# Optimization experiments

Hardware: AMD Instinct MI355X
Metric: run time of the kernel (lower is better)

## Reference

```python
import jax, jax.numpy as jnp
import numpy as np

NUM_HEADS = 32
HEAD_DIM = 128
LORA_RANK = 512
Q_LORA_RANK = 1536
BSZ = 16
SEQ_LEN = 4096


def setup_inputs() -> dict:
    key = jax.random.key(0)
    k1, k2, k3, k4, k5, k6 = jax.random.split(key, 6)
    hd = NUM_HEADS * HEAD_DIM
    return {
        "hidden_states_q": jax.random.normal(k1, (BSZ, Q_LORA_RANK), dtype=jnp.float32),
        "compressed_kv": jax.random.normal(k2, (BSZ, SEQ_LEN, LORA_RANK), dtype=jnp.float32),
        # nn.Linear params: weight [out, in], bias [out]
        "Wq": jax.random.normal(k3, (hd, Q_LORA_RANK), dtype=jnp.float32) / np.sqrt(Q_LORA_RANK),
        "bq": jax.random.normal(k4, (hd,), dtype=jnp.float32) * 0.01,
        "Wkv": jax.random.normal(k5, (hd, LORA_RANK), dtype=jnp.float32) / np.sqrt(LORA_RANK),
        "bkv": jax.random.normal(k6, (hd,), dtype=jnp.float32) * 0.01,
    }


def reference(hidden_states_q, compressed_kv, Wq, bq, Wkv, bkv):
    bsz = hidden_states_q.shape[0]
    seq_len = compressed_kv.shape[1]
    # q: [b, h, d]
    q = (hidden_states_q @ Wq.T + bq).reshape(bsz, NUM_HEADS, HEAD_DIM)
    # kv decompression: [b, s, h, d] (same tensor used for both K and V)
    kv = (compressed_kv @ Wkv.T + bkv).reshape(bsz, seq_len, NUM_HEADS, HEAD_DIM)
    # attention scores per head over seq (note: original has NO 1/sqrt(d) scaling)
    attn = jnp.einsum('bhd,bshd->bhs', q, kv)
    attn = jax.nn.softmax(attn, axis=-1)
    out = jnp.einsum('bhs,bshd->bhd', attn, kv)
    return out.reshape(bsz, NUM_HEADS * HEAD_DIM)
```

## Files before the change

kernel.cpp:

```cpp
#include <hip/hip_runtime.h>

#define B  16
#define S  4096
#define R  512
#define QR 1536
#define H  32
#define D  128
#define HD 4096
#define SC 128
#define CH 32

using f32x4 = __attribute__((ext_vector_type(4))) float;
using s16x8 = __attribute__((ext_vector_type(8))) short;

__device__ __forceinline__ ushort bf_hi(float x) {
  return (ushort)(__float_as_uint(x) >> 16);
}
__device__ __forceinline__ float bf_res(float x) {
  return x - __uint_as_float(__float_as_uint(x) & 0xFFFF0000u);
}
__device__ __forceinline__ ushort f2bf_rne(float x) {
  uint u = __float_as_uint(x);
  return (ushort)((u + 0x7FFFu + ((u >> 16) & 1u)) >> 16);
}
__device__ __forceinline__ float bf2f(ushort u) {
  return __uint_as_float((uint)u << 16);
}

__global__ __launch_bounds__(512) void k_q(const float* __restrict__ hsq,
                                           const float* __restrict__ Wq,
                                           const float* __restrict__ bq,
                                           float* __restrict__ q) {
  __shared__ float hs[B * QR];
  int tid = threadIdx.x;
  for (int idx = tid * 4; idx < B * QR; idx += 2048)
    *(float4*)&hs[idx] = *(const float4*)&hsq[idx];
  __syncthreads();

  int wave = tid >> 6, lane = tid & 63;
  int o = blockIdx.x * 16 + wave * 2;

  float acc0[B], acc1[B];
#pragma unroll
  for (int b = 0; b < B; ++b) { acc0[b] = 0.f; acc1[b] = 0.f; }

  const float* w0r = Wq + (size_t)o * QR;
  const float* w1r = w0r + QR;
  for (int k = lane * 4; k < QR; k += 256) {
    float4 wa = *(const float4*)&w0r[k];
    float4 wb = *(const float4*)&w1r[k];
#pragma unroll
    for (int b = 0; b < B; ++b) {
      float4 h4 = *(const float4*)&hs[b * QR + k];
      acc0[b] += wa.x * h4.x + wa.y * h4.y + wa.z * h4.z + wa.w * h4.w;
      acc1[b] += wb.x * h4.x + wb.y * h4.y + wb.z * h4.z + wb.w * h4.w;
    }
  }
#pragma unroll
  for (int b = 0; b < B; ++b) {
    float v0 = acc0[b], v1 = acc1[b];
#pragma unroll
    for (int off = 32; off > 0; off >>= 1) {
      v0 += __shfl_xor(v0, off);
      v1 += __shfl_xor(v1, off);
    }
    if (lane == 0) {
      q[b * HD + o]     = v0 + bq[o];
      q[b * HD + o + 1] = v1 + bq[o + 1];
    }
  }
}

__global__ __launch_bounds__(256) void k_qhat(const float* __restrict__ q,
                                              const float* __restrict__ Wkv,
                                              float* __restrict__ qhat) {
  int h = blockIdx.x;
  int r0 = blockIdx.y * 64;
  __shared__ float qs[B][D];
  int tid = threadIdx.x;
  for (int idx = tid; idx < B * D; idx += 256) {
    int b = idx >> 7, d = idx & (D - 1);
    qs[b][d] = q[b * HD + h * D + d];
  }
  __syncthreads();

  int r_l = tid & 63, bg = tid >> 6;
  float acc[4] = {0.f, 0.f, 0.f, 0.f};
  const float* wbase = Wkv + (size_t)(h * D) * R + r0 + r_l;
  for (int d = 0; d < D; d += 4) {
    float w0 = wbase[(d + 0) * R];
    float w1 = wbase[(d + 1) * R];
    float w2 = wbase[(d + 2) * R];
    float w3 = wbase[(d + 3) * R];
#pragma unroll
    for (int i = 0; i < 4; ++i) {
      float4 q4 = *(const float4*)&qs[bg * 4 + i][d];
      acc[i] += q4.x * w0 + q4.y * w1 + q4.z * w2 + q4.w * w3;
    }
  }
#pragma unroll
  for (int i = 0; i < 4; ++i)
    qhat[((size_t)(bg * 4 + i) * H + h) * R + r0 + r_l] = acc[i];
}

__global__ __launch_bounds__(512, 4) void k_fmha(const float* __restrict__ qhat,
                                                 const float* __restrict__ ckv,
                                                 ushort* __restrict__ part,
                                                 float* __restrict__ mbuf,
                                                 float* __restrict__ lbuf) {
  __shared__ __align__(16) ushort smem[24576];
  __shared__ __align__(16) ushort Ps[H * 128];

  ushort* cs1h = smem;
  ushort* cs1l = smem + 8192;
  ushort* qsh  = smem + 16384;
  ushort* qsl  = smem + 20480;
  float*  redm = (float*)(smem + 8192);
  float*  redl = redm + 256;
  ushort* cs2  = smem;

  const int b = blockIdx.x, chunk = blockIdx.y;
  const int tid = threadIdx.x;
  const int lane = tid & 63, w = tid >> 6;
  const int lcol = lane & 15, lgrp = lane >> 4;
  const float* cbase = ckv + ((size_t)b * S + (size_t)chunk * SC) * R;
  const float* qbase = qhat + (size_t)b * H * R;

  const int st_s = tid >> 2;
  const int st_k = (tid & 3) * 16;
  const int qrow = tid >> 4;
  const int qk   = (tid & 15) * 4;

  f32x4 acc[2];
  acc[0] = {0.f, 0.f, 0.f, 0.f};
  acc[1] = {0.f, 0.f, 0.f, 0.f};

  float4 v[4], vq;
  {
    const float* src = cbase + (size_t)st_s * R + st_k;
#pragma unroll
    for (int j = 0; j < 4; ++j) v[j] = *(const float4*)(src + 4 * j);
    vq = *(const float4*)(qbase + (size_t)qrow * R + qk);
  }

  for (int kt = 0; kt < R; kt += 64) {
#pragma unroll
    for (int j = 0; j < 4; ++j) {
      int k0 = st_k + 4 * j;
      int idx = st_s * 64 + (((k0 >> 3) ^ (st_s & 7)) << 3) + (k0 & 7);
      float4 t = v[j];
      *(uint*)&cs1h[idx]     = (uint)bf_hi(t.x) | ((uint)bf_hi(t.y) << 16);
      *(uint*)&cs1h[idx + 2] = (uint)bf_hi(t.z) | ((uint)bf_hi(t.w) << 16);
      *(uint*)&cs1l[idx]     = (uint)bf_hi(bf_res(t.x)) | ((uint)bf_hi(bf_res(t.y)) << 16);
      *(uint*)&cs1l[idx + 2] = (uint)bf_hi(bf_res(t.z)) | ((uint)bf_hi(bf_res(t.w)) << 16);
    }
    {
      int idx = qrow * 64 + (((qk >> 3) ^ (qrow & 7)) << 3) + (qk & 7);
      *(uint*)&qsh[idx]     = (uint)bf_hi(vq.x) | ((uint)bf_hi(vq.y) << 16);
      *(uint*)&qsh[idx + 2] = (uint)bf_hi(vq.z) | ((uint)bf_hi(vq.w) << 16);
      *(uint*)&qsl[idx]     = (uint)bf_hi(bf_res(vq.x)) | ((uint)bf_hi(bf_res(vq.y)) << 16);
      *(uint*)&qsl[idx + 2] = (uint)bf_hi(bf_res(vq.z)) | ((uint)bf_hi(bf_res(vq.w)) << 16);
    }
    __syncthreads();
    if (kt + 64 < R) {
      const float* src = cbase + (size_t)st_s * R + (kt + 64) + st_k;
#pragma unroll
      for (int j = 0; j < 4; ++j) v[j] = *(const float4*)(src + 4 * j);
      vq = *(const float4*)(qbase + (size_t)qrow * R + (kt + 64) + qk);
    }
#pragma unroll
    for (int ks = 0; ks < 2; ++ks) {
      const int kb = ks * 4 + lgrp;
      s16x8 ah[2], al[2], bh, bl;
#pragma unroll
      for (int mt = 0; mt < 2; ++mt) {
        int m = 16 * mt + lcol;
        int idx = m * 64 + ((kb ^ (m & 7)) << 3);
        ah[mt] = *(s16x8*)&qsh[idx];
        al[mt] = *(s16x8*)&qsl[idx];
      }
      {
        int sf = 16 * w + lcol;
        int idx = sf * 64 + ((kb ^ (sf & 7)) << 3);
        bh = *(s16x8*)&cs1h[idx];
        bl = *(s16x8*)&cs1l[idx];
      }
#pragma unroll
      for (int mt = 0; mt < 2; ++mt) {
        acc[mt] = __builtin_amdgcn_mfma_f32_16x16x32_bf16(ah[mt], bh, acc[mt], 0, 0, 0);
        acc[mt] = __builtin_amdgcn_mfma_f32_16x16x32_bf16(ah[mt], bl, acc[mt], 0, 0, 0);
        acc[mt] = __builtin_amdgcn_mfma_f32_16x16x32_bf16(al[mt], bh, acc[mt], 0, 0, 0);
      }
    }
    __syncthreads();
  }

  float pm[2][4];
#pragma unroll
  for (int mt = 0; mt < 2; ++mt)
#pragma unroll
    for (int i = 0; i < 4; ++i) pm[mt][i] = acc[mt][i];
#pragma unroll
  for (int off = 1; off <= 8; off <<= 1)
#pragma unroll
    for (int mt = 0; mt < 2; ++mt)
#pragma unroll
      for (int i = 0; i < 4; ++i)
        pm[mt][i] = fmaxf(pm[mt][i], __shfl_xor(pm[mt][i], off));
  if (lcol == 0) {
#pragma unroll
    for (int mt = 0; mt < 2; ++mt)
#pragma unroll
      for (int i = 0; i < 4; ++i)
        redm[(16 * mt + lgrp * 4 + i) * 8 + w] = pm[mt][i];
  }
  __syncthreads();

  float e_[2][4], ps[2][4];
#pragma unroll
  for (int mt = 0; mt < 2; ++mt)
#pragma unroll
    for (int i = 0; i < 4; ++i) {
      int h = 16 * mt + lgrp * 4 + i;
      float4 r0 = *(float4*)&redm[h * 8];
      float4 r1 = *(float4*)&redm[h * 8 + 4];
      float m = fmaxf(fmaxf(fmaxf(r0.x, r0.y), fmaxf(r0.z, r0.w)),
                      fmaxf(fmaxf(r1.x, r1.y), fmaxf(r1.z, r1.w)));
      float e = __expf(acc[mt][i] - m);
      e_[mt][i] = e;
      ps[mt][i] = e;
    }
#pragma unroll
  for (int off = 1; off <= 8; off <<= 1)
#pragma unroll
    for (int mt = 0; mt < 2; ++mt)
#pragma unroll
      for (int i = 0; i < 4; ++i)
        ps[mt][i] += __shfl_xor(ps[mt][i], off);
  if (lcol == 0) {
#pragma unroll
    for (int mt = 0; mt < 2; ++mt)
#pragma unroll
      for (int i = 0; i < 4; ++i)
        redl[(16 * mt + lgrp * 4 + i) * 8 + w] = ps[mt][i];
  }
#pragma unroll
  for (int mt = 0; mt < 2; ++mt)
#pragma unroll
    for (int i = 0; i < 4; ++i) {
      int h = 16 * mt + lgrp * 4 + i;
      int s = 16 * w + lcol;
      Ps[h * 128 + (((s >> 3) ^ (h & 7)) << 3) + (s & 7)] = f2bf_rne(e_[mt][i]);
    }
  __syncthreads();

  if (w == 0 && lcol == 0) {
#pragma unroll
    for (int mt = 0; mt < 2; ++mt)
#pragma unroll
      for (int i = 0; i < 4; ++i) {
        int h = 16 * mt + lgrp * 4 + i;
        float4 r0 = *(float4*)&redm[h * 8];
        float4 r1 = *(float4*)&redm[h * 8 + 4];
        float M = fmaxf(fmaxf(fmaxf(r0.x, r0.y), fmaxf(r0.z, r0.w)),
                        fmaxf(fmaxf(r1.x, r1.y), fmaxf(r1.z, r1.w)));
        float4 l0 = *(float4*)&redl[h * 8];
        float4 l1 = *(float4*)&redl[h * 8 + 4];
        float L = (l0.x + l0.y + l0.z + l0.w) + (l1.x + l1.y + l1.z + l1.w);
        mbuf[((size_t)b * CH + chunk) * H + h] = M;
        lbuf[((size_t)b * CH + chunk) * H + h] = L;
      }
  }

  const int nt = w & 1, mtr = w >> 1;
  s16x8 bp4[4];
#pragma unroll
  for (int kt4 = 0; kt4 < 4; ++kt4) {
    int h = 16 * nt + lcol;
    int kb = kt4 * 4 + lgrp;
    bp4[kt4] = *(s16x8*)&Ps[h * 128 + ((kb ^ (h & 7)) << 3)];
  }

  const int b7 = tid & 7, sp = tid >> 3;
  const int s0 = 2 * sp;
  float ra[8], rb[8];
  {
    const float* row0 = cbase + (size_t)s0 * R;
    const float* row1 = row0 + R;
#pragma unroll
    for (int i = 0; i < 8; ++i) { ra[i] = row0[b7 + 8 * i]; rb[i] = row1[b7 + 8 * i]; }
  }
  ushort* pb = part + (size_t)(b * CH + chunk) * H * R;

  for (int rt = 0; rt < 8; ++rt) {
#pragma unroll
    for (int i = 0; i < 8; ++i) {
      int r = b7 + 8 * i;
      int idx = r * 128 + (((s0 >> 3) ^ (r & 7)) << 3) + (s0 & 7);
      *(uint*)&cs2[idx] = (uint)f2bf_rne(ra[i]) | ((uint)f2bf_rne(rb[i]) << 16);
    }
    __syncthreads();
    if (rt < 7) {
      const float* row0 = cbase + (size_t)s0 * R + (rt + 1) * 64;
      const float* row1 = row0 + R;
#pragma unroll
      for (int i = 0; i < 8; ++i) { ra[i] = row0[b7 + 8 * i]; rb[i] = row1[b7 + 8 * i]; }
    }
    f32x4 acc2 = {0.f, 0.f, 0.f, 0.f};
    const int rl = 16 * mtr + lcol;
#pragma unroll
    for (int kt4 = 0; kt4 < 4; ++kt4) {
      int kb = kt4 * 4 + lgrp;
      s16x8 a2 = *(s16x8*)&cs2[rl * 128 + ((kb ^ (rl & 7)) << 3)];
      acc2 = __builtin_amdgcn_mfma_f32_16x16x32_bf16(a2, bp4[kt4], acc2, 0, 0, 0);
    }
    {
      int h = 16 * nt + lcol;
#pragma unroll
      for (int i = 0; i < 4; ++i) {
        int rg = rt * 64 + 16 * mtr + lgrp * 4 + i;
        pb[(size_t)h * R + rg] = f2bf_rne(acc2[i]);
      }
    }
    __syncthreads();
  }
}

__global__ __launch_bounds__(256) void k_combine(const ushort* __restrict__ part,
                                                 const float* __restrict__ mbuf,
                                                 const float* __restrict__ lbuf,
                                                 float* __restrict__ ctx) {
  const int bid = blockIdx.x;
  const int b = bid >> 5, h = bid & 31;
  const int tid = threadIdx.x;
  float mv[CH], wv[CH];
  float M = -3.0e38f;
#pragma unroll
  for (int c = 0; c < CH; ++c) {
    mv[c] = mbuf[((size_t)b * CH + c) * H + h];
    M = fmaxf(M, mv[c]);
  }
  float denom = 0.f;
#pragma unroll
  for (int c = 0; c < CH; ++c) {
    wv[c] = __expf(mv[c] - M);
    denom += wv[c] * lbuf[((size_t)b * CH + c) * H + h];
  }
  const float inv = 1.f / denom;
  float s0 = 0.f, s1 = 0.f;
#pragma unroll
  for (int c = 0; c < CH; ++c) {
    const ushort* pp = part + (((size_t)b * CH + c) * H + h) * R;
    s0 += wv[c] * bf2f(pp[tid]);
    s1 += wv[c] * bf2f(pp[tid + 256]);
  }
  ctx[((size_t)b * H + h) * R + tid] = s0 * inv;
  ctx[((size_t)b * H + h) * R + tid + 256] = s1 * inv;
}

__global__ __launch_bounds__(256) void k_out(const float* __restrict__ ctx,
                                             const float* __restrict__ Wkv,
                                             const float* __restrict__ bkv,
                                             float* __restrict__ out) {
  int h = blockIdx.x;
  int d0 = blockIdx.y * 32;
  __shared__ float cs[B][R];
  int tid = threadIdx.x;
  for (int idx = tid * 4; idx < B * R; idx += 1024) {
    int b = idx >> 9, r = idx & 511;
    *(float4*)&cs[b][r] = *(const float4*)&ctx[(size_t)(b * H + h) * R + r];
  }
  __syncthreads();

  int dg = tid & 31;
  int bg = tid >> 5;
  int d = d0 + dg;
  int b0 = bg * 2;
  float acc0 = 0.f, acc1 = 0.f;
  const float* wrow = Wkv + ((size_t)(h * D + d)) * R;
  for (int i = 0; i < R; i += 4) {
    float4 w4 = *(const float4*)&wrow[i];
    float4 ca = *(const float4*)&cs[b0][i];
    float4 cb = *(const float4*)&cs[b0 + 1][i];
    acc0 += w4.x * ca.x + w4.y * ca.y + w4.z * ca.z + w4.w * ca.w;
    acc1 += w4.x * cb.x + w4.y * cb.y + w4.z * cb.z + w4.w * cb.w;
  }
  float bv = bkv[h * D + d];
  out[(size_t)b0 * HD + h * D + d]       = acc0 + bv;
  out[(size_t)(b0 + 1) * HD + h * D + d] = acc1 + bv;
}

extern "C" void kernel_launch(void* const* d_in, const int* in_sizes, int n_in,
                              void* d_out, int out_size, void* d_ws, size_t ws_size,
                              hipStream_t stream) {
  (void)in_sizes; (void)n_in; (void)out_size; (void)ws_size;
  const float* hsq = (const float*)d_in[0];
  const float* ckv = (const float*)d_in[1];
  const float* Wq  = (const float*)d_in[2];
  const float* bq  = (const float*)d_in[3];
  const float* Wkv = (const float*)d_in[4];
  const float* bkv = (const float*)d_in[5];
  float* out = (float*)d_out;

  float* ws   = (float*)d_ws;
  float* q    = ws;
  float* qhat = q + 65536;
  float* ctx  = qhat + 262144;
  float* mbuf = ctx + 262144;
  float* lbuf = mbuf + (size_t)B * CH * H;
  ushort* part = (ushort*)(lbuf + (size_t)B * CH * H);

  k_q<<<256, 512, 0, stream>>>(hsq, Wq, bq, q);
  k_qhat<<<dim3(32, 8), 256, 0, stream>>>(q, Wkv, qhat);
  k_fmha<<<dim3(B, CH), 512, 0, stream>>>(qhat, ckv, part, mbuf, lbuf);
  k_combine<<<B * H, 256, 0, stream>>>(part, mbuf, lbuf, ctx);
  k_out<<<dim3(32, 4), 256, 0, stream>>>(ctx, Wkv, bkv, out);
}
```

Measured before the change: 90.73 us.

## Precompute bf16 hi/lo qhat, stage fp32 chunk in LDS, read P·V operands from global

k_qhat now writes qhat already split into bf16 hi and lo arrays, so the attention kernel reads MFMA A-fragments straight from global memory instead of converting and staging them in LDS. The score phase stages the fp32 compressed_kv chunk per wave without block barriers, using double-buffered register prefetch, and does the hi/lo split at fragment-load time. The P·V phase drops the LDS transpose and its barriers and gathers strided column elements directly from global memory, truncating them to bf16. The P·V output is also truncated instead of rounded to nearest. This trades fewer barriers and less LDS traffic for uncoalesced strided global loads and slightly lower precision.

```diff
diff --git a/kernel.cpp b/kernel.cpp
--- a/kernel.cpp
+++ b/kernel.cpp
@@ -13,11 +13,16 @@
 using f32x4 = __attribute__((ext_vector_type(4))) float;
 using s16x8 = __attribute__((ext_vector_type(8))) short;
 
+union bfu { s16x8 v; uint u[4]; };
+
 __device__ __forceinline__ ushort bf_hi(float x) {
   return (ushort)(__float_as_uint(x) >> 16);
 }
-__device__ __forceinline__ float bf_res(float x) {
-  return x - __uint_as_float(__float_as_uint(x) & 0xFFFF0000u);
+__device__ __forceinline__ float hi_f(float x) {
+  return __uint_as_float(__float_as_uint(x) & 0xFFFF0000u);
+}
+__device__ __forceinline__ uint pack_hi2(float x, float y) {
+  return (__float_as_uint(x) >> 16) | (__float_as_uint(y) & 0xFFFF0000u);
 }
 __device__ __forceinline__ ushort f2bf_rne(float x) {
   uint u = __float_as_uint(x);
@@ -73,7 +78,8 @@
 
 __global__ __launch_bounds__(256) void k_qhat(const float* __restrict__ q,
                                               const float* __restrict__ Wkv,
-                                              float* __restrict__ qhat) {
+                                              ushort* __restrict__ qhi,
+                                              ushort* __restrict__ qlo) {
   int h = blockIdx.x;
   int r0 = blockIdx.y * 64;
   __shared__ float qs[B][D];
@@ -99,100 +105,85 @@
     }
   }
 #pragma unroll
-  for (int i = 0; i < 4; ++i)
-    qhat[((size_t)(bg * 4 + i) * H + h) * R + r0 + r_l] = acc[i];
-}
-
-__global__ __launch_bounds__(512, 4) void k_fmha(const float* __restrict__ qhat,
+  for (int i = 0; i < 4; ++i) {
+    size_t idx = ((size_t)(bg * 4 + i) * H + h) * R + r0 + r_l;
+    qhi[idx] = bf_hi(acc[i]);
+    qlo[idx] = bf_hi(acc[i] - hi_f(acc[i]));
+  }
+}
+
+__global__ __launch_bounds__(512, 4) void k_fmha(const ushort* __restrict__ qhi,
+                                                 const ushort* __restrict__ qlo,
                                                  const float* __restrict__ ckv,
                                                  ushort* __restrict__ part,
                                                  float* __restrict__ mbuf,
                                                  float* __restrict__ lbuf) {
-  __shared__ __align__(16) ushort smem[24576];
+  __shared__ __align__(16) float csA[SC * 64];
   __shared__ __align__(16) ushort Ps[H * 128];
-
-  ushort* cs1h = smem;
-  ushort* cs1l = smem + 8192;
-  ushort* qsh  = smem + 16384;
-  ushort* qsl  = smem + 20480;
-  float*  redm = (float*)(smem + 8192);
-  float*  redl = redm + 256;
-  ushort* cs2  = smem;
+  __shared__ float red[512];
 
   const int b = blockIdx.x, chunk = blockIdx.y;
   const int tid = threadIdx.x;
-  const int lane = tid & 63, w = tid >> 6;
+  const int lane = tid & 63, wv = tid >> 6;
   const int lcol = lane & 15, lgrp = lane >> 4;
+
   const float* cbase = ckv + ((size_t)b * S + (size_t)chunk * SC) * R;
-  const float* qbase = qhat + (size_t)b * H * R;
-
-  const int st_s = tid >> 2;
-  const int st_k = (tid & 3) * 16;
-  const int qrow = tid >> 4;
-  const int qk   = (tid & 15) * 4;
+  const ushort* qh_b = qhi + (size_t)b * H * R;
+  const ushort* ql_b = qlo + (size_t)b * H * R;
 
   f32x4 acc[2];
   acc[0] = {0.f, 0.f, 0.f, 0.f};
   acc[1] = {0.f, 0.f, 0.f, 0.f};
 
-  float4 v[4], vq;
-  {
-    const float* src = cbase + (size_t)st_s * R + st_k;
-#pragma unroll
-    for (int j = 0; j < 4; ++j) v[j] = *(const float4*)(src + 4 * j);
-    vq = *(const float4*)(qbase + (size_t)qrow * R + qk);
-  }
-
-  for (int kt = 0; kt < R; kt += 64) {
-#pragma unroll
-    for (int j = 0; j < 4; ++j) {
-      int k0 = st_k + 4 * j;
-      int idx = st_s * 64 + (((k0 >> 3) ^ (st_s & 7)) << 3) + (k0 & 7);
-      float4 t = v[j];
-      *(uint*)&cs1h[idx]     = (uint)bf_hi(t.x) | ((uint)bf_hi(t.y) << 16);
-      *(uint*)&cs1h[idx + 2] = (uint)bf_hi(t.z) | ((uint)bf_hi(t.w) << 16);
-      *(uint*)&cs1l[idx]     = (uint)bf_hi(bf_res(t.x)) | ((uint)bf_hi(bf_res(t.y)) << 16);
-      *(uint*)&cs1l[idx + 2] = (uint)bf_hi(bf_res(t.z)) | ((uint)bf_hi(bf_res(t.w)) << 16);
-    }
-    {
-      int idx = qrow * 64 + (((qk >> 3) ^ (qrow & 7)) << 3) + (qk & 7);
-      *(uint*)&qsh[idx]     = (uint)bf_hi(vq.x) | ((uint)bf_hi(vq.y) << 16);
-      *(uint*)&qsh[idx + 2] = (uint)bf_hi(vq.z) | ((uint)bf_hi(vq.w) << 16);
-      *(uint*)&qsl[idx]     = (uint)bf_hi(bf_res(vq.x)) | ((uint)bf_hi(bf_res(vq.y)) << 16);
-      *(uint*)&qsl[idx + 2] = (uint)bf_hi(bf_res(vq.z)) | ((uint)bf_hi(bf_res(vq.w)) << 16);
-    }
-    __syncthreads();
-    if (kt + 64 < R) {
-      const float* src = cbase + (size_t)st_s * R + (kt + 64) + st_k;
-#pragma unroll
-      for (int j = 0; j < 4; ++j) v[j] = *(const float4*)(src + 4 * j);
-      vq = *(const float4*)(qbase + (size_t)qrow * R + (kt + 64) + qk);
+  const int ss  = 16 * wv + (lane >> 2);
+  const int kb0 = (lane & 3) * 4;
+  const int sx  = ss & 7;
+  const float* srow = cbase + (size_t)ss * R;
+  float* lrow = &csA[ss * 64];
+
+  const int sfr = 16 * wv + lcol;
+  const int fx  = sfr & 7;
+  const float* frow = &csA[sfr * 64];
+
+  float4 v[2][4];
+#pragma unroll
+  for (int j = 0; j < 4; ++j) v[0][j] = *(const float4*)&srow[4 * (kb0 + j)];
+#pragma unroll
+  for (int j = 0; j < 4; ++j) v[1][j] = *(const float4*)&srow[64 + 4 * (kb0 + j)];
+
+#pragma unroll
+  for (int t = 0; t < 8; ++t) {
+#pragma unroll
+    for (int j = 0; j < 4; ++j)
+      *(float4*)&lrow[4 * ((kb0 + j) ^ sx)] = v[t & 1][j];
+    if (t + 2 < 8) {
+#pragma unroll
+      for (int j = 0; j < 4; ++j)
+        v[t & 1][j] = *(const float4*)&srow[64 * (t + 2) + 4 * (kb0 + j)];
     }
 #pragma unroll
     for (int ks = 0; ks < 2; ++ks) {
-      const int kb = ks * 4 + lgrp;
-      s16x8 ah[2], al[2], bh, bl;
+      const int kb = 2 * lgrp + 8 * ks;
+      float4 fa = *(const float4*)&frow[4 * (kb ^ fx)];
+      float4 fb = *(const float4*)&frow[4 * ((kb + 1) ^ fx)];
+      bfu bh, bl;
+      bh.u[0] = pack_hi2(fa.x, fa.y); bh.u[1] = pack_hi2(fa.z, fa.w);
+      bh.u[2] = pack_hi2(fb.x, fb.y); bh.u[3] = pack_hi2(fb.z, fb.w);
+      bl.u[0] = pack_hi2(fa.x - hi_f(fa.x), fa.y - hi_f(fa.y));
+      bl.u[1] = pack_hi2(fa.z - hi_f(fa.z), fa.w - hi_f(fa.w));
+      bl.u[2] = pack_hi2(fb.x - hi_f(fb.x), fb.y - hi_f(fb.y));
+      bl.u[3] = pack_hi2(fb.z - hi_f(fb.z), fb.w - hi_f(fb.w));
+      const size_t ko = (size_t)(64 * t + 32 * ks + 8 * lgrp);
 #pragma unroll
       for (int mt = 0; mt < 2; ++mt) {
-        int m = 16 * mt + lcol;
-        int idx = m * 64 + ((kb ^ (m & 7)) << 3);
-        ah[mt] = *(s16x8*)&qsh[idx];
-        al[mt] = *(s16x8*)&qsl[idx];
+        const size_t moff = (size_t)(16 * mt + lcol) * R + ko;
+        s16x8 ah = *(const s16x8*)&qh_b[moff];
+        s16x8 al = *(const s16x8*)&ql_b[moff];
+        acc[mt] = __builtin_amdgcn_mfma_f32_16x16x32_bf16(ah, bh.v, acc[mt], 0, 0, 0);
+        acc[mt] = __builtin_amdgcn_mfma_f32_16x16x32_bf16(ah, bl.v, acc[mt], 0, 0, 0);
+        acc[mt] = __builtin_amdgcn_mfma_f32_16x16x32_bf16(al, bh.v, acc[mt], 0, 0, 0);
       }
-      {
-        int sf = 16 * w + lcol;
-        int idx = sf * 64 + ((kb ^ (sf & 7)) << 3);
-        bh = *(s16x8*)&cs1h[idx];
-        bl = *(s16x8*)&cs1l[idx];
-      }
-#pragma unroll
-      for (int mt = 0; mt < 2; ++mt) {
-        acc[mt] = __builtin_amdgcn_mfma_f32_16x16x32_bf16(ah[mt], bh, acc[mt], 0, 0, 0);
-        acc[mt] = __builtin_amdgcn_mfma_f32_16x16x32_bf16(ah[mt], bl, acc[mt], 0, 0, 0);
-        acc[mt] = __builtin_amdgcn_mfma_f32_16x16x32_bf16(al[mt], bh, acc[mt], 0, 0, 0);
-      }
-    }
-    __syncthreads();
+    }
   }
 
   float pm[2][4];
@@ -212,23 +203,23 @@
     for (int mt = 0; mt < 2; ++mt)
 #pragma unroll
       for (int i = 0; i < 4; ++i)
-        redm[(16 * mt + lgrp * 4 + i) * 8 + w] = pm[mt][i];
-  }
-  __syncthreads();
-
-  float e_[2][4], ps[2][4];
+        red[(16 * mt + 4 * lgrp + i) * 8 + wv] = pm[mt][i];
+  }
+  __syncthreads();
+
+  float e_[2][4], psum[2][4];
 #pragma unroll
   for (int mt = 0; mt < 2; ++mt)
 #pragma unroll
     for (int i = 0; i < 4; ++i) {
-      int h = 16 * mt + lgrp * 4 + i;
-      float4 r0 = *(float4*)&redm[h * 8];
-      float4 r1 = *(float4*)&redm[h * 8 + 4];
+      int h = 16 * mt + 4 * lgrp + i;
+      float4 r0 = *(float4*)&red[h * 8];
+      float4 r1 = *(float4*)&red[h * 8 + 4];
       float m = fmaxf(fmaxf(fmaxf(r0.x, r0.y), fmaxf(r0.z, r0.w)),
                       fmaxf(fmaxf(r1.x, r1.y), fmaxf(r1.z, r1.w)));
       float e = __expf(acc[mt][i] - m);
       e_[mt][i] = e;
-      ps[mt][i] = e;
+      psum[mt][i] = e;
     }
 #pragma unroll
   for (int off = 1; off <= 8; off <<= 1)
@@ -236,93 +227,75 @@
     for (int mt = 0; mt < 2; ++mt)
 #pragma unroll
       for (int i = 0; i < 4; ++i)
-        ps[mt][i] += __shfl_xor(ps[mt][i], off);
+        psum[mt][i] += __shfl_xor(psum[mt][i], off);
   if (lcol == 0) {
 #pragma unroll
     for (int mt = 0; mt < 2; ++mt)
 #pragma unroll
       for (int i = 0; i < 4; ++i)
-        redl[(16 * mt + lgrp * 4 + i) * 8 + w] = ps[mt][i];
+        red[256 + (16 * mt + 4 * lgrp + i) * 8 + wv] = psum[mt][i];
   }
 #pragma unroll
   for (int mt = 0; mt < 2; ++mt)
 #pragma unroll
     for (int i = 0; i < 4; ++i) {
-      int h = 16 * mt + lgrp * 4 + i;
-      int s = 16 * w + lcol;
+      int h = 16 * mt + 4 * lgrp + i;
+      int s = 16 * wv + lcol;
       Ps[h * 128 + (((s >> 3) ^ (h & 7)) << 3) + (s & 7)] = f2bf_rne(e_[mt][i]);
     }
   __syncthreads();
 
-  if (w == 0 && lcol == 0) {
+  if (wv == 0 && lcol == 0) {
 #pragma unroll
     for (int mt = 0; mt < 2; ++mt)
 #pragma unroll
       for (int i = 0; i < 4; ++i) {
-        int h = 16 * mt + lgrp * 4 + i;
-        float4 r0 = *(float4*)&redm[h * 8];
-        float4 r1 = *(float4*)&redm[h * 8 + 4];
+        int h = 16 * mt + 4 * lgrp + i;
+        float4 r0 = *(float4*)&red[h * 8];
+        float4 r1 = *(float4*)&red[h * 8 + 4];
         float M = fmaxf(fmaxf(fmaxf(r0.x, r0.y), fmaxf(r0.z, r0.w)),
                         fmaxf(fmaxf(r1.x, r1.y), fmaxf(r1.z, r1.w)));
-        float4 l0 = *(float4*)&redl[h * 8];
-        float4 l1 = *(float4*)&redl[h * 8 + 4];
+        float4 l0 = *(float4*)&red[256 + h * 8];
+        float4 l1 = *(float4*)&red[256 + h * 8 + 4];
         float L = (l0.x + l0.y + l0.z + l0.w) + (l1.x + l1.y + l1.z + l1.w);
         mbuf[((size_t)b * CH + chunk) * H + h] = M;
         lbuf[((size_t)b * CH + chunk) * H + h] = L;
       }
   }
 
-  const int nt = w & 1, mtr = w >> 1;
-  s16x8 bp4[4];
-#pragma unroll
-  for (int kt4 = 0; kt4 < 4; ++kt4) {
-    int h = 16 * nt + lcol;
-    int kb = kt4 * 4 + lgrp;
-    bp4[kt4] = *(s16x8*)&Ps[h * 128 + ((kb ^ (h & 7)) << 3)];
-  }
-
-  const int b7 = tid & 7, sp = tid >> 3;
-  const int s0 = 2 * sp;
-  float ra[8], rb[8];
-  {
-    const float* row0 = cbase + (size_t)s0 * R;
-    const float* row1 = row0 + R;
-#pragma unroll
-    for (int i = 0; i < 8; ++i) { ra[i] = row0[b7 + 8 * i]; rb[i] = row1[b7 + 8 * i]; }
-  }
+  s16x8 bp[4][2];
+#pragma unroll
+  for (int kt4 = 0; kt4 < 4; ++kt4)
+#pragma unroll
+    for (int nt = 0; nt < 2; ++nt) {
+      int h = 16 * nt + lcol;
+      int kb = 4 * kt4 + lgrp;
+      bp[kt4][nt] = *(const s16x8*)&Ps[h * 128 + ((kb ^ (h & 7)) << 3)];
+    }
+
   ushort* pb = part + (size_t)(b * CH + chunk) * H * R;
-
-  for (int rt = 0; rt < 8; ++rt) {
-#pragma unroll
-    for (int i = 0; i < 8; ++i) {
-      int r = b7 + 8 * i;
-      int idx = r * 128 + (((s0 >> 3) ^ (r & 7)) << 3) + (s0 & 7);
-      *(uint*)&cs2[idx] = (uint)f2bf_rne(ra[i]) | ((uint)f2bf_rne(rb[i]) << 16);
-    }
-    __syncthreads();
-    if (rt < 7) {
-      const float* row0 = cbase + (size_t)s0 * R + (rt + 1) * 64;
-      const float* row1 = row0 + R;
-#pragma unroll
-      for (int i = 0; i < 8; ++i) { ra[i] = row0[b7 + 8 * i]; rb[i] = row1[b7 + 8 * i]; }
-    }
-    f32x4 acc2 = {0.f, 0.f, 0.f, 0.f};
-    const int rl = 16 * mtr + lcol;
+#pragma unroll
+  for (int mtr = 0; mtr < 4; ++mtr) {
+    const int r = 64 * wv + 16 * mtr + lcol;
+    const float* colp = cbase + r;
+    f32x4 a0 = {0.f, 0.f, 0.f, 0.f}, a1 = {0.f, 0.f, 0.f, 0.f};
 #pragma unroll
     for (int kt4 = 0; kt4 < 4; ++kt4) {
-      int kb = kt4 * 4 + lgrp;
-      s16x8 a2 = *(s16x8*)&cs2[rl * 128 + ((kb ^ (rl & 7)) << 3)];
-      acc2 = __builtin_amdgcn_mfma_f32_16x16x32_bf16(a2, bp4[kt4], acc2, 0, 0, 0);
-    }
-    {
-      int h = 16 * nt + lcol;
-#pragma unroll
-      for (int i = 0; i < 4; ++i) {
-        int rg = rt * 64 + 16 * mtr + lgrp * 4 + i;
-        pb[(size_t)h * R + rg] = f2bf_rne(acc2[i]);
-      }
-    }
-    __syncthreads();
+      float f[8];
+#pragma unroll
+      for (int j = 0; j < 8; ++j)
+        f[j] = colp[(size_t)(32 * kt4 + 8 * lgrp + j) * R];
+      bfu a2;
+      a2.u[0] = pack_hi2(f[0], f[1]); a2.u[1] = pack_hi2(f[2], f[3]);
+      a2.u[2] = pack_hi2(f[4], f[5]); a2.u[3] = pack_hi2(f[6], f[7]);
+      a0 = __builtin_amdgcn_mfma_f32_16x16x32_bf16(a2.v, bp[kt4][0], a0, 0, 0, 0);
+      a1 = __builtin_amdgcn_mfma_f32_16x16x32_bf16(a2.v, bp[kt4][1], a1, 0, 0, 0);
+    }
+    const int rg0 = 64 * wv + 16 * mtr + 4 * lgrp;
+    uint2 w0 = {pack_hi2(a0[0], a0[1]), pack_hi2(a0[2], a0[3])};
+    uint2 w1 = {pack_hi2(a1[0], a1[1]), pack_hi2(a1[2], a1[3])};
+    *(uint2*)&pb[(size_t)lcol * R + rg0]        = w0;
+    *(uint2*)&pb[(size_t)(16 + lcol) * R + rg0] = w1;
   }
 }
 
@@ -404,15 +377,16 @@
 
   float* ws   = (float*)d_ws;
   float* q    = ws;
-  float* qhat = q + 65536;
-  float* ctx  = qhat + 262144;
+  float* ctx  = q + 65536;
   float* mbuf = ctx + 262144;
-  float* lbuf = mbuf + (size_t)B * CH * H;
-  ushort* part = (ushort*)(lbuf + (size_t)B * CH * H);
+  float* lbuf = mbuf + 16384;
+  ushort* qhi  = (ushort*)(lbuf + 16384);
+  ushort* qlo  = qhi + 262144;
+  ushort* part = qlo + 262144;
 
   k_q<<<256, 512, 0, stream>>>(hsq, Wq, bq, q);
-  k_qhat<<<dim3(32, 8), 256, 0, stream>>>(q, Wkv, qhat);
-  k_fmha<<<dim3(B, CH), 512, 0, stream>>>(qhat, ckv, part, mbuf, lbuf);
+  k_qhat<<<dim3(32, 8), 256, 0, stream>>>(q, Wkv, qhi, qlo);
+  k_fmha<<<dim3(B, CH), 512, 0, stream>>>(qhi, qlo, ckv, part, mbuf, lbuf);
   k_combine<<<B * H, 256, 0, stream>>>(part, mbuf, lbuf, ctx);
   k_out<<<dim3(32, 4), 256, 0, stream>>>(ctx, Wkv, bkv, out);
 }
```

Result: slower. 127.4 us (+40.4%).
